# Performance work log

Hardware: AMD Instinct MI355X
Metric: run time of the kernel (lower is better)

Reference implementation:

```python
import jax, jax.numpy as jnp
import numpy as np

B, N, H = 8, 2000, 64  # batch, num_nodes(=input_dim), hidden(num_gru_units)


def _laplacian_self_loop(a):
    # batched: norm = D^{-1/2} (A + I) D^{-1/2}
    m = a + jnp.eye(a.shape[-1], dtype=a.dtype)
    d_inv_sqrt = jnp.sum(m, axis=-1) ** -0.5  # (B, N)
    return d_inv_sqrt[..., :, None] * m * d_inv_sqrt[..., None, :]


def _graph_conv(inputs, hidden_flat, adj, windd, W2, b2, W3, b3, W, b, out_dim):
    b_, _, n = inputs.shape
    # dynamic wind-based adjacency
    wind_now = inputs[:, 2, :] * 360.0  # (B, N)
    direction = jnp.abs(windd[None, :, :] - wind_now[:, :, None])  # (B, N, N)
    direction = jnp.where(direction > 360.0, 180.0, direction)
    d1 = jnp.maximum(jnp.cos(direction * (jnp.pi / 180.0)), 0.0)
    a = d1 @ W2.T + b2 + (adj @ W3.T + b3)[None]  # (B, N, N)
    a1 = _laplacian_self_loop(jnp.maximum(a, 0.0))
    # graph conv: concat [x, h] then A @ [.] then Linear
    x = jnp.concatenate([inputs[:, 0, :, None], hidden_flat.reshape(b_, n, H)], axis=2)  # (B,N,H+1)
    y = jnp.einsum('bij,bjh->bih', a1, x) @ W.T + b  # (B, N, out_dim)
    return y.reshape(b_, n * out_dim)


def reference(inputs, hidden_state, adj, windd, W2, b2, W3, b3, W1a, b1a, W1b, b1b, Wca1, Wca2, Wsa):
    b_, _, n = inputs.shape
    conc = _graph_conv(inputs, hidden_state, adj, windd, W2, b2, W3, b3, W1a, b1a, 2 * H)
    conc = conc.reshape(b_, 2 * H, n)  # faithful reshape (input_dim == N)
    # --- channel attention (CBAM) ---
    avg = jnp.mean(conc, axis=2, keepdims=True)  # (B, 2H, 1)
    mx = jnp.max(conc, axis=2, keepdims=True)
    def fc(v):
        return jnp.einsum('oc,bcx->box', Wca2, jax.nn.relu(jnp.einsum('oc,bcx->box', Wca1, v)))
    ca = jax.nn.sigmoid(fc(avg) + fc(mx))  # (B, 2H, 1)
    conc = ca * conc
    # --- spatial attention ---
    s = jnp.stack([jnp.mean(conc, axis=1), jnp.max(conc, axis=1)], axis=1)  # (B, 2, N)
    sa = jax.lax.conv_general_dilated(s, Wsa, window_strides=(1,), padding=((3, 3),),
                                      dimension_numbers=('NCH', 'OIH', 'NCH'))  # (B,1,N)
    conc = jax.nn.sigmoid(sa) * conc
    # --- GRU gates ---
    conc = jax.nn.sigmoid(conc.reshape(b_, 2 * H * n))
    r, u = jnp.split(conc, 2, axis=1)  # each (B, N*H)
    c = jnp.tanh(_graph_conv(inputs, r * hidden_state, adj, windd, W2, b2, W3, b3, W1b, b1b, H))
    new_hidden_state = u * hidden_state + (1.0 - u) * c
    return new_hidden_state


def setup_inputs() -> dict:
    key = jax.random.key(0)
    ks = jax.random.split(key, 12)
    inputs = jax.random.uniform(ks[0], (B, 3, N), dtype=jnp.float32)
    hidden_state = jax.random.normal(ks[1], (B, N * H), dtype=jnp.float32) * 0.1
    adj = jax.random.uniform(ks[2], (N, N), dtype=jnp.float32)
    windd = jax.random.uniform(ks[3], (N, N), dtype=jnp.float32) * 360.0
    sN = 1.0 / np.sqrt(N)
    W2 = jax.random.normal(ks[4], (N, N), dtype=jnp.float32) * sN
    b2 = jnp.zeros((N,), jnp.float32)
    W3 = jax.random.normal(ks[5], (N, N), dtype=jnp.float32) * sN
    b3 = jnp.zeros((N,), jnp.float32)
    sI = 1.0 / np.sqrt(H + 1)
    W1a = jax.random.normal(ks[6], (2 * H, H + 1), dtype=jnp.float32) * sI
    b1a = jnp.ones((2 * H,), jnp.float32)  # bias=1.0 in graph_conv1
    W1b = jax.random.normal(ks[7], (H, H + 1), dtype=jnp.float32) * sI
    b1b = jnp.zeros((H,), jnp.float32)
    Wca1 = jax.random.normal(ks[8], (2 * H // 16, 2 * H), dtype=jnp.float32) * (1.0 / np.sqrt(2 * H))
    Wca2 = jax.random.normal(ks[9], (2 * H, 2 * H // 16), dtype=jnp.float32) * (1.0 / np.sqrt(2 * H // 16))
    Wsa = jax.random.normal(ks[10], (1, 2, 7), dtype=jnp.float32) * (1.0 / np.sqrt(14))
    return {'inputs': inputs, 'hidden_state': hidden_state, 'adj': adj, 'windd': windd,
            'W2': W2, 'b2': b2, 'W3': W3, 'b3': b3, 'W1a': W1a, 'b1a': b1a,
            'W1b': W1b, 'b1b': b1b, 'Wca1': Wca1, 'Wca2': Wca2, 'Wsa': Wsa}
```

## Files before the change

kernel.cpp:

```cpp
#include <hip/hip_runtime.h>

#define NN 2000
#define BB 8
#define P  2048
#define NIT 32

typedef __attribute__((ext_vector_type(8))) short bf16x8;
typedef __attribute__((ext_vector_type(4))) float f32x4;

__device__ __forceinline__ float sigf(float x) { return 1.0f / (1.0f + expf(-x)); }

__device__ __forceinline__ short f2bf(float x) {
    union { float f; unsigned u; } v; v.f = x;
    unsigned r = v.u + 0x7fffu + ((v.u >> 16) & 1u);
    return (short)(r >> 16);
}
__device__ __forceinline__ float bf2f(short h) {
    union { unsigned u; float f; } v; v.u = ((unsigned)(unsigned short)h) << 16; return v.f;
}

__device__ __forceinline__ void gl2lds16(const short* g, short* l) {
    __builtin_amdgcn_global_load_lds(
        (const __attribute__((address_space(1))) void*)g,
        (__attribute__((address_space(3))) void*)l, 16, 0, 0);
}

__global__ __launch_bounds__(256) void k_cvtW(
    const float* __restrict__ s0, const float* __restrict__ s1, const float* __restrict__ s2,
    short* __restrict__ d0, short* __restrict__ d1, short* __restrict__ d2)
{
    const int i = blockIdx.x, sel = blockIdx.y, t = threadIdx.x;
    const float* s = (sel == 0) ? s0 : (sel == 1) ? s1 : s2;
    short* d = ((sel == 0) ? d0 : (sel == 1) ? d1 : d2) + ((size_t)i) * P + t * 8;
    bf16x8 v;
#pragma unroll
    for (int e = 0; e < 8; ++e) v[e] = 0;
    if (i < NN && t < 250) {
        const float* p = s + (size_t)i * NN + t * 8;
        float4 x0 = *(const float4*)p;
        float4 x1 = *(const float4*)(p + 4);
        float a[8] = {x0.x,x0.y,x0.z,x0.w,x1.x,x1.y,x1.z,x1.w};
#pragma unroll
        for (int e = 0; e < 8; ++e) v[e] = f2bf(a[e]);
    }
    *(bf16x8*)d = v;
}

__global__ __launch_bounds__(256) void k_cvtD1(
    const float* __restrict__ windd, const float* __restrict__ inputs, short* __restrict__ d1bf)
{
    const int i = blockIdx.x, t = threadIdx.x;
    const bool live = (i < NN) && (t < 250);
    float a[8];
    if (live) {
        const float* p = windd + (size_t)i * NN + t * 8;
        float4 x0 = *(const float4*)p;
        float4 x1 = *(const float4*)(p + 4);
        a[0]=x0.x; a[1]=x0.y; a[2]=x0.z; a[3]=x0.w;
        a[4]=x1.x; a[5]=x1.y; a[6]=x1.z; a[7]=x1.w;
    }
#pragma unroll
    for (int b = 0; b < BB; ++b) {
        bf16x8 v;
#pragma unroll
        for (int e = 0; e < 8; ++e) v[e] = 0;
        if (live) {
            const float wn = inputs[(size_t)b * 3 * NN + 2 * NN + i] * 360.0f;
#pragma unroll
            for (int e = 0; e < 8; ++e) {
                float dd = fabsf(a[e] - wn);
                dd = (dd > 360.0f) ? 180.0f : dd;
                float c = __cosf(dd * 0.01745329251994329577f);
                v[e] = f2bf(fmaxf(c, 0.0f));
            }
        }
        *(bf16x8*)(d1bf + ((size_t)b * P + i) * P + t * 8) = v;
    }
}

__global__ __launch_bounds__(512, 2) void k_gd(
    const short* __restrict__ d1bf, const short* __restrict__ W2bf,
    const float* __restrict__ b2, const short* __restrict__ adjw,
    short* __restrict__ m_bf)
{
    __shared__ char smem[131072];
    const int t = threadIdx.x;
    const int w = t >> 6, lane = t & 63;
    const int wm = w >> 2, wn = w & 3;
    const int lr = lane & 15, lq = lane >> 4;
    const int tile = blockIdx.x;
    const int b = blockIdx.y;
    const int i0 = (tile & 7) * 256;
    const int j0 = (tile >> 3) * 256;
    const short* A  = d1bf + (size_t)b * P * P;
    const short* Bm = W2bf;

    const short* srcA[4];
    const short* srcB[4];
#pragma unroll
    for (int q = 0; q < 4; ++q) {
        const int c = q * 512 + t;
        const int r = c >> 3;
        const int g = (c & 7) ^ (r & 7);
        srcA[q] = A  + (size_t)(i0 + r) * P + g * 8;
        srcB[q] = Bm + (size_t)(j0 + r) * P + g * 8;
    }

#define STAGE_ALL(slot, ktI) do {                                                      \
        gl2lds16(srcA[0] + (ktI) * 64, (short*)(smem + (slot) * 32768 + (w * 64) * 16));          \
        gl2lds16(srcA[1] + (ktI) * 64, (short*)(smem + (slot) * 32768 + (512 + w * 64) * 16));    \
        gl2lds16(srcA[2] + (ktI) * 64, (short*)(smem + (slot) * 32768 + (1024 + w * 64) * 16));   \
        gl2lds16(srcA[3] + (ktI) * 64, (short*)(smem + (slot) * 32768 + (1536 + w * 64) * 16));   \
        gl2lds16(srcB[0] + (ktI) * 64, (short*)(smem + 65536 + (slot) * 32768 + (w * 64) * 16));          \
        gl2lds16(srcB[1] + (ktI) * 64, (short*)(smem + 65536 + (slot) * 32768 + (512 + w * 64) * 16));    \
        gl2lds16(srcB[2] + (ktI) * 64, (short*)(smem + 65536 + (slot) * 32768 + (1024 + w * 64) * 16));   \
        gl2lds16(srcB[3] + (ktI) * 64, (short*)(smem + 65536 + (slot) * 32768 + (1536 + w * 64) * 16)); } while (0)

    const int fx0 = (lq << 4) ^ ((lr & 7) << 4);
    const int fx1 = ((4 + lq) << 4) ^ ((lr & 7) << 4);
    const int arowB = (wm * 128 + lr) * 128;
    const int browB = (wn * 64 + lr) * 128;

    f32x4 acc[8][4];
#pragma unroll
    for (int m = 0; m < 8; ++m)
#pragma unroll
        for (int n = 0; n < 4; ++n) acc[m][n] = (f32x4){0.f, 0.f, 0.f, 0.f};
    bf16x8 aF[4][2], bF[4][2];

    STAGE_ALL(0, 0);
    asm volatile("s_waitcnt vmcnt(0)" ::: "memory");
    __builtin_amdgcn_s_barrier();
    asm volatile("" ::: "memory");

#define MFMA_(a_, b_, m, n) acc[m][n] = __builtin_amdgcn_mfma_f32_16x16x32_bf16(a_, b_, acc[m][n], 0, 0, 0)

    for (int kt = 0; kt < NIT; ++kt) {
        char* curA = smem + (kt & 1) * 32768;
        char* curB = smem + 65536 + (kt & 1) * 32768;
        const int stgSlot = (kt + 1) & 1;
        const int stgKt = (kt + 1 < NIT) ? (kt + 1) : (NIT - 1);

        STAGE_ALL(stgSlot, stgKt);

#pragma unroll
        for (int m = 0; m < 4; ++m) {
            aF[m][0] = *(const bf16x8*)(curA + arowB + m * 2048 + fx0);
            aF[m][1] = *(const bf16x8*)(curA + arowB + m * 2048 + fx1);
        }
#pragma unroll
        for (int n = 0; n < 4; ++n) {
            bF[n][0] = *(const bf16x8*)(curB + browB + n * 2048 + fx0);
            bF[n][1] = *(const bf16x8*)(curB + browB + n * 2048 + fx1);
        }
        asm volatile("s_waitcnt lgkmcnt(0)" ::: "memory");
        __builtin_amdgcn_sched_barrier(0);
        __builtin_amdgcn_s_setprio(1);
#pragma unroll
        for (int m = 0; m < 4; ++m)
#pragma unroll
            for (int n = 0; n < 4; ++n) {
                MFMA_(aF[m][0], bF[n][0], m, n);
                MFMA_(aF[m][1], bF[n][1], m, n);
            }
        __builtin_amdgcn_s_setprio(0);

#pragma unroll
        for (int m = 0; m < 4; ++m) {
            aF[m][0] = *(const bf16x8*)(curA + arowB + (m + 4) * 2048 + fx0);
            aF[m][1] = *(const bf16x8*)(curA + arowB + (m + 4) * 2048 + fx1);
        }
        asm volatile("s_waitcnt lgkmcnt(0)" ::: "memory");
        __builtin_amdgcn_sched_barrier(0);
        __builtin_amdgcn_s_setprio(1);
#pragma unroll
        for (int m = 0; m < 4; ++m)
#pragma unroll
            for (int n = 0; n < 4; ++n) {
                MFMA_(aF[m][0], bF[n][0], m + 4, n);
                MFMA_(aF[m][1], bF[n][1], m + 4, n);
            }
        __builtin_amdgcn_s_setprio(0);

        asm volatile("s_waitcnt vmcnt(0)" ::: "memory");
        __builtin_amdgcn_s_barrier();
        asm volatile("" ::: "memory");
    }

    const int rbase = i0 + wm * 128 + lq * 4;
    const int cbase = j0 + wn * 64 + lr;
#pragma unroll
    for (int m = 0; m < 8; ++m) {
#pragma unroll
        for (int n = 0; n < 4; ++n) {
            const int col = cbase + n * 16;
#pragma unroll
            for (int q = 0; q < 4; ++q) {
                const int row = rbase + m * 16 + q;
                short o = 0;
                if (row < NN && col < NN) {
                    float x = acc[m][n][q] + b2[col] + bf2f(adjw[(size_t)row * NN + col]);
                    x = fmaxf(x, 0.0f);
                    if (row == col) x += 1.0f;
                    o = f2bf(x);
                }
                m_bf[((size_t)b * P + row) * P + col] = o;
            }
        }
    }
#undef MFMA_
#undef STAGE_ALL
}

template<int EPI, int OUTD>
__global__ __launch_bounds__(256) void k_mfma(
    const short* __restrict__ Abase, const short* __restrict__ Bbase,
    const float* __restrict__ bias, const short* __restrict__ adjw,
    void* __restrict__ Cout, short* __restrict__ part, size_t aBatch)
{
    __shared__ short shA[4096];
    __shared__ short shB[4096];
    const int t = threadIdx.x;
    const int w = t >> 6, lane = t & 63;
    const int wr = w >> 1, wc = w & 1;

    int i0, j0, b, kt = 0;
    if (EPI == 2) {
        i0 = blockIdx.x * 128; j0 = 0; kt = blockIdx.y; b = blockIdx.z;
    } else {
        i0 = blockIdx.x * 128; j0 = blockIdx.y * 128; b = 0;
    }
    const int kb = (EPI == 2) ? kt * (P / 4) : 0;
    const int ke = (EPI == 2) ? kt * (P / 4) + (P / 4) : P;

    const short* A  = Abase + (size_t)b * aBatch;
    const short* Bm = Bbase + ((EPI == 2) ? (size_t)b * 128 * P : (size_t)0);

    f32x4 acc[4][4];
#pragma unroll
    for (int m = 0; m < 4; ++m)
#pragma unroll
        for (int n = 0; n < 4; ++n) acc[m][n] = (f32x4){0.f, 0.f, 0.f, 0.f};

    const int lidx0 = w * 128 + lane;
    const int lidx1 = lidx0 + 64;
    const short* aS0 = A  + (size_t)(i0 + (lidx0 >> 2)) * P + (lidx0 & 3) * 8;
    const short* aS1 = A  + (size_t)(i0 + (lidx1 >> 2)) * P + (lidx1 & 3) * 8;
    const short* bS0 = Bm + (size_t)(j0 + (lidx0 >> 2)) * P + (lidx0 & 3) * 8;
    const short* bS1 = Bm + (size_t)(j0 + (lidx1 >> 2)) * P + (lidx1 & 3) * 8;
    short* ldA0 = shA + (w * 128) * 8;
    short* ldA1 = shA + (w * 128 + 64) * 8;
    short* ldB0 = shB + (w * 128) * 8;
    short* ldB1 = shB + (w * 128 + 64) * 8;

    const int lr = lane & 15, lq = lane >> 4;
    const int aoff = (wr * 64 + lr) * 32 + lq * 8;
    const int boff = (wc * 64 + lr) * 32 + lq * 8;

    for (int k0 = kb; k0 < ke; k0 += 32) {
        gl2lds16(aS0 + k0, ldA0);
        gl2lds16(aS1 + k0, ldA1);
        gl2lds16(bS0 + k0, ldB0);
        gl2lds16(bS1 + k0, ldB1);
        __syncthreads();
        bf16x8 aF[4], bF[4];
#pragma unroll
        for (int m = 0; m < 4; ++m) aF[m] = *(const bf16x8*)(shA + aoff + m * 512);
#pragma unroll
        for (int n = 0; n < 4; ++n) bF[n] = *(const bf16x8*)(shB + boff + n * 512);
#pragma unroll
        for (int m = 0; m < 4; ++m)
#pragma unroll
            for (int n = 0; n < 4; ++n)
                acc[m][n] = __builtin_amdgcn_mfma_f32_16x16x32_bf16(aF[m], bF[n], acc[m][n], 0, 0, 0);
        __syncthreads();
    }

    const int rbase = i0 + wr * 64 + lq * 4;
    const int cbase = j0 + wc * 64 + lr;
#pragma unroll
    for (int m = 0; m < 4; ++m) {
#pragma unroll
        for (int n = 0; n < 4; ++n) {
            const int col = cbase + n * 16;
#pragma unroll
            for (int q = 0; q < 4; ++q) {
                const int row = rbase + m * 16 + q;
                float v = acc[m][n][q];
                if (EPI == 0) {
                    if (row < NN && col < NN)
                        ((short*)Cout)[(size_t)row * NN + col] = f2bf(v + bias[col]);
                } else {
                    if (row < NN && col < OUTD)
                        part[((size_t)(kt * BB + b) * NN + row) * OUTD + col] = f2bf(v);
                }
            }
        }
    }
}

template<int OUTD>
__global__ __launch_bounds__(256) void k_comb(
    const short* __restrict__ part, const float* __restrict__ dinv,
    const float* __restrict__ bias, float* __restrict__ out)
{
    const size_t idx = (size_t)blockIdx.x * 256 + threadIdx.x;
    const size_t S = (size_t)BB * NN * OUTD;
    if (idx >= S) return;
    const int o = (int)(idx % OUTD);
    const size_t r = idx / OUTD;
    const int i = (int)(r % NN);
    const int b = (int)(r / NN);
    float s = (bf2f(part[idx]) + bf2f(part[idx + S])) +
              (bf2f(part[idx + 2 * S]) + bf2f(part[idx + 3 * S]));
    out[idx] = s * dinv[b * NN + i] + bias[o];
}

__global__ __launch_bounds__(256) void k_cfin(
    const short* __restrict__ part, const float* __restrict__ dinv,
    const float* __restrict__ bias, const float* __restrict__ u,
    const float* __restrict__ hidden, float* __restrict__ out)
{
    const size_t idx = (size_t)blockIdx.x * 256 + threadIdx.x;
    const size_t S = (size_t)BB * NN * 64;
    if (idx >= S) return;
    const int o = (int)(idx & 63);
    const size_t r = idx >> 6;
    const int i = (int)(r % NN);
    const int b = (int)(r / NN);
    float s = (bf2f(part[idx]) + bf2f(part[idx + S])) +
              (bf2f(part[idx + 2 * S]) + bf2f(part[idx + 3 * S]));
    float c = tanhf(s * dinv[b * NN + i] + bias[o]);
    float uu = u[idx];
    out[idx] = uu * hidden[idx] + (1.0f - uu) * c;
}

__global__ __launch_bounds__(256) void k_rowsum_bf(const short* __restrict__ m_bf, float* __restrict__ dinv)
{
    const int i = blockIdx.x, b = blockIdx.y;
    const short* p = m_bf + ((size_t)b * P + i) * P + threadIdx.x * 8;
    bf16x8 v = *(const bf16x8*)p;
    float s = 0.0f;
#pragma unroll
    for (int e = 0; e < 8; ++e) s += bf2f(v[e]);
#pragma unroll
    for (int off = 32; off > 0; off >>= 1) s += __shfl_down(s, off);
    __shared__ float red[4];
    if ((threadIdx.x & 63) == 0) red[threadIdx.x >> 6] = s;
    __syncthreads();
    if (threadIdx.x == 0) dinv[b * NN + i] = rsqrtf(red[0] + red[1] + red[2] + red[3]);
}

template<int OUT>
__global__ __launch_bounds__(128) void k_xwT(
    const float* __restrict__ inputs, const float* __restrict__ hsrc,
    const float* __restrict__ W, const float* __restrict__ dinv, short* __restrict__ zT)
{
    const int b = blockIdx.y;
    const int j0 = blockIdx.x * 16;
    const int t = threadIdx.x;
    __shared__ float wl[128 * 65];
    __shared__ float xs[16 * 66];
    __shared__ float dj[16];
    for (int idx = t; idx < OUT * 65; idx += 128) wl[idx] = W[idx];
    for (int idx = t; idx < 16 * 64; idx += 128) {
        int jj = idx >> 6, hh = idx & 63, j = j0 + jj;
        xs[jj * 66 + 1 + hh] = (j < NN) ? hsrc[((size_t)b * NN + j) * 64 + hh] : 0.0f;
    }
    if (t < 16) {
        int j = j0 + t;
        xs[t * 66] = (j < NN) ? inputs[(size_t)b * 3 * NN + j] : 0.0f;
        dj[t] = (j < NN) ? dinv[b * NN + j] : 0.0f;
    }
    __syncthreads();
    for (int jj = 0; jj < 16; ++jj) {
        float a = 0.0f;
        if (t < OUT) {
            const float* xr = &xs[jj * 66];
            const float* wr = &wl[t * 65];
#pragma unroll
            for (int c = 0; c < 65; ++c) a = fmaf(xr[c], wr[c], a);
        }
        int j = j0 + jj;
        zT[((size_t)b * 128 + t) * P + j] = (t < OUT && j < NN) ? f2bf(a * dj[jj]) : (short)0;
    }
}

__global__ __launch_bounds__(256) void k_chred(const float* __restrict__ conc,
                                               float* __restrict__ avg, float* __restrict__ mx)
{
    const int bc = blockIdx.x;
    const float* p = conc + (size_t)bc * NN;
    float s = 0.0f, mv = -3.402823466e+38f;
    for (int n = threadIdx.x; n < NN; n += 256) { float v = p[n]; s += v; mv = fmaxf(mv, v); }
#pragma unroll
    for (int off = 32; off > 0; off >>= 1) {
        s += __shfl_down(s, off);
        mv = fmaxf(mv, __shfl_down(mv, off));
    }
    __shared__ float rs[4], rm[4];
    if ((threadIdx.x & 63) == 0) { rs[threadIdx.x >> 6] = s; rm[threadIdx.x >> 6] = mv; }
    __syncthreads();
    if (threadIdx.x == 0) {
        avg[bc] = (rs[0] + rs[1] + rs[2] + rs[3]) * (1.0f / NN);
        mx[bc]  = fmaxf(fmaxf(rm[0], rm[1]), fmaxf(rm[2], rm[3]));
    }
}

__global__ __launch_bounds__(128) void k_ca(
    const float* __restrict__ avg, const float* __restrict__ mx,
    const float* __restrict__ Wca1, const float* __restrict__ Wca2, float* __restrict__ ca)
{
    const int b = blockIdx.x, t = threadIdx.x;
    __shared__ float av[128], mv[128], h[16];
    av[t] = avg[b * 128 + t];
    mv[t] = mx[b * 128 + t];
    __syncthreads();
    if (t < 16) {
        int o8 = t & 7;
        const float* src = (t < 8) ? av : mv;
        float s = 0.0f;
        for (int c = 0; c < 128; ++c) s = fmaf(Wca1[o8 * 128 + c], src[c], s);
        h[t] = fmaxf(s, 0.0f);
    }
    __syncthreads();
    float s = 0.0f;
#pragma unroll
    for (int k = 0; k < 8; ++k) s = fmaf(Wca2[t * 8 + k], h[k] + h[8 + k], s);
    ca[b * 128 + t] = sigf(s);
}

__global__ __launch_bounds__(256) void k_satgate(
    const float* __restrict__ conc, const float* __restrict__ ca,
    const float* __restrict__ Wsa, const float* __restrict__ hidden,
    float* __restrict__ rh, float* __restrict__ u)
{
    const int b = blockIdx.y;
    const int n0 = blockIdx.x * 256;
    const int t = threadIdx.x;
    __shared__ float cas[128];
    __shared__ float wsa[14];
    __shared__ float s0l[262], s1l[262];
    if (t < 128) cas[t] = ca[b * 128 + t];
    if (t >= 128 && t < 142) wsa[t - 128] = Wsa[t - 128];
    __syncthreads();

    const float* cb = conc + (size_t)b * NN * 128;
    {
        const int n = n0 + t;
        float sm = 0.0f, sx = -3.402823466e+38f;
        if (n < NN) {
            for (int c = 0; c < 128; ++c) {
                float v = cas[c] * cb[(size_t)c * NN + n];
                sm += v; sx = fmaxf(sx, v);
            }
            s0l[t + 3] = sm * (1.0f / 128.0f);
            s1l[t + 3] = sx;
        } else { s0l[t + 3] = 0.0f; s1l[t + 3] = 0.0f; }
    }
    if (t < 6) {
        const int hn = (t < 3) ? (n0 - 3 + t) : (n0 + 256 + (t - 3));
        const int hi = (t < 3) ? t : (256 + t);
        float sm = 0.0f, sx = -3.402823466e+38f;
        if (hn >= 0 && hn < NN) {
            for (int c = 0; c < 128; ++c) {
                float v = cas[c] * cb[(size_t)c * NN + hn];
                sm += v; sx = fmaxf(sx, v);
            }
            s0l[hi] = sm * (1.0f / 128.0f);
            s1l[hi] = sx;
        } else { s0l[hi] = 0.0f; s1l[hi] = 0.0f; }
    }
    __syncthreads();

    const int n = n0 + t;
    if (n >= NN) return;
    float sa = 0.0f;
#pragma unroll
    for (int k = 0; k < 7; ++k)
        sa += wsa[k] * s0l[t + k] + wsa[7 + k] * s1l[t + k];
    float gs = sigf(sa);
    for (int c = 0; c < 128; ++c) {
        float v = gs * cas[c] * cb[(size_t)c * NN + n];
        float g = sigf(v);
        if (c < 64)
            rh[(size_t)b * NN * 64 + (size_t)c * NN + n] =
                g * hidden[(size_t)b * NN * 64 + (size_t)c * NN + n];
        else
            u[(size_t)b * NN * 64 + (size_t)(c - 64) * NN + n] = g;
    }
}

extern "C" void kernel_launch(void* const* d_in, const int* in_sizes, int n_in,
                              void* d_out, int out_size, void* d_ws, size_t ws_size,
                              hipStream_t stream)
{
    (void)in_sizes; (void)n_in; (void)out_size; (void)ws_size;
    const float* inputs = (const float*)d_in[0];
    const float* hidden = (const float*)d_in[1];
    const float* adj    = (const float*)d_in[2];
    const float* windd  = (const float*)d_in[3];
    const float* W2     = (const float*)d_in[4];
    const float* b2     = (const float*)d_in[5];
    const float* W3     = (const float*)d_in[6];
    const float* b3     = (const float*)d_in[7];
    const float* W1a    = (const float*)d_in[8];
    const float* b1a    = (const float*)d_in[9];
    const float* W1b    = (const float*)d_in[10];
    const float* b1b    = (const float*)d_in[11];
    const float* Wca1   = (const float*)d_in[12];
    const float* Wca2   = (const float*)d_in[13];
    const float* Wsa    = (const float*)d_in[14];
    float* out = (float*)d_out;

    char* W = (char*)d_ws;
    short* adjW3bf = (short*)(W + 0);
    short* W2bf    = (short*)(W + 8000000);
    short* W3bf    = (short*)(W + 16388608);
    short* adjbf   = (short*)(W + 24777216);
    short* m_bf    = (short*)(W + 16388608);
    char* D = W + 83497472;
    short* d1bf = (short*)D;
    float* dinv = (float*)(D + 0);
    float* avgb = (float*)(D + 64000);
    float* mxb  = (float*)(D + 68096);
    float* cab  = (float*)(D + 72192);
    short* zT   = (short*)(D + 204800);
    float* conc = (float*)(D + 4399104);
    float* rh   = (float*)(D + 12591104);
    float* ubuf = (float*)(D + 16687104);
    short* part = (short*)(D + 24879104);

    const size_t PP = (size_t)P * P;

    k_cvtW<<<dim3(P, 3), 256, 0, stream>>>(W2, W3, adj, W2bf, W3bf, adjbf);
    k_cvtD1<<<P, 256, 0, stream>>>(windd, inputs, d1bf);
    k_mfma<0, 0><<<dim3(16, 16, 1), 256, 0, stream>>>(adjbf, W3bf, b3, nullptr, adjW3bf, nullptr, 0);
    k_gd<<<dim3(64, BB), 512, 0, stream>>>(d1bf, W2bf, b2, adjW3bf, m_bf);
    k_rowsum_bf<<<dim3(NN, BB), 256, 0, stream>>>(m_bf, dinv);
    k_xwT<128><<<dim3(128, BB), 128, 0, stream>>>(inputs, hidden, W1a, dinv, zT);
    k_mfma<2, 128><<<dim3(16, 4, BB), 256, 0, stream>>>(m_bf, zT, nullptr, nullptr, nullptr, part, PP);
    k_comb<128><<<(BB * NN * 128 + 255) / 256, 256, 0, stream>>>(part, dinv, b1a, conc);
    k_chred<<<BB * 128, 256, 0, stream>>>(conc, avgb, mxb);
    k_ca<<<BB, 128, 0, stream>>>(avgb, mxb, Wca1, Wca2, cab);
    k_satgate<<<dim3(8, BB), 256, 0, stream>>>(conc, cab, Wsa, hidden, rh, ubuf);
    k_xwT<64><<<dim3(128, BB), 128, 0, stream>>>(inputs, rh, W1b, dinv, zT);
    k_mfma<2, 64><<<dim3(16, 4, BB), 256, 0, stream>>>(m_bf, zT, nullptr, nullptr, nullptr, part, PP);
    k_cfin<<<(BB * NN * 64 + 255) / 256, 256, 0, stream>>>(part, dinv, b1b, ubuf, hidden, out);
}
```

Measured before the change: 411.9 us.

## Restructure dynamic-adjacency GEMM into four-stage K=32 LDS pipeline with prefetch depth two

The main batched d1@W2 GEMM kernel now uses K-tiles of 32 instead of 64, with four LDS slots and loads issued two tiles ahead. Each iteration waits only on the older tile's loads (vmcnt(4)) rather than draining all outstanding loads. This is meant to hide global-to-LDS latency behind the MFMA work. The cost is twice as many barriers per K, a new swizzle pattern and more live fragment registers (8 A fragments at once).

```diff
diff --git a/kernel.cpp b/kernel.cpp
--- a/kernel.cpp
+++ b/kernel.cpp
@@ -3,7 +3,7 @@
 #define NN 2000
 #define BB 8
 #define P  2048
-#define NIT 32
+#define NIT4 64
 
 typedef __attribute__((ext_vector_type(8))) short bf16x8;
 typedef __attribute__((ext_vector_type(4))) float f32x4;
@@ -78,7 +78,7 @@
     }
 }
 
-__global__ __launch_bounds__(512, 2) void k_gd(
+__global__ __launch_bounds__(512, 2) void k_gq(
     const short* __restrict__ d1bf, const short* __restrict__ W2bf,
     const float* __restrict__ b2, const short* __restrict__ adjw,
     short* __restrict__ m_bf)
@@ -95,97 +95,62 @@
     const short* A  = d1bf + (size_t)b * P * P;
     const short* Bm = W2bf;
 
-    const short* srcA[4];
-    const short* srcB[4];
-#pragma unroll
-    for (int q = 0; q < 4; ++q) {
-        const int c = q * 512 + t;
-        const int r = c >> 3;
-        const int g = (c & 7) ^ (r & 7);
-        srcA[q] = A  + (size_t)(i0 + r) * P + g * 8;
-        srcB[q] = Bm + (size_t)(j0 + r) * P + g * 8;
-    }
-
-#define STAGE_ALL(slot, ktI) do {                                                      \
-        gl2lds16(srcA[0] + (ktI) * 64, (short*)(smem + (slot) * 32768 + (w * 64) * 16));          \
-        gl2lds16(srcA[1] + (ktI) * 64, (short*)(smem + (slot) * 32768 + (512 + w * 64) * 16));    \
-        gl2lds16(srcA[2] + (ktI) * 64, (short*)(smem + (slot) * 32768 + (1024 + w * 64) * 16));   \
-        gl2lds16(srcA[3] + (ktI) * 64, (short*)(smem + (slot) * 32768 + (1536 + w * 64) * 16));   \
-        gl2lds16(srcB[0] + (ktI) * 64, (short*)(smem + 65536 + (slot) * 32768 + (w * 64) * 16));          \
-        gl2lds16(srcB[1] + (ktI) * 64, (short*)(smem + 65536 + (slot) * 32768 + (512 + w * 64) * 16));    \
-        gl2lds16(srcB[2] + (ktI) * 64, (short*)(smem + 65536 + (slot) * 32768 + (1024 + w * 64) * 16));   \
-        gl2lds16(srcB[3] + (ktI) * 64, (short*)(smem + 65536 + (slot) * 32768 + (1536 + w * 64) * 16)); } while (0)
-
-    const int fx0 = (lq << 4) ^ ((lr & 7) << 4);
-    const int fx1 = ((4 + lq) << 4) ^ ((lr & 7) << 4);
-    const int arowB = (wm * 128 + lr) * 128;
-    const int browB = (wn * 64 + lr) * 128;
+    const int c0 = t,       r0 = c0 >> 2;
+    const int c1 = 512 + t, r1 = c1 >> 2;
+    const int g0 = (c0 & 3) ^ ((r0 >> 1) & 3);
+    const int g1 = (c1 & 3) ^ ((r1 >> 1) & 3);
+    const short* srcA0 = A  + (size_t)(i0 + r0) * P + g0 * 8;
+    const short* srcA1 = A  + (size_t)(i0 + r1) * P + g1 * 8;
+    const short* srcB0 = Bm + (size_t)(j0 + r0) * P + g0 * 8;
+    const short* srcB1 = Bm + (size_t)(j0 + r1) * P + g1 * 8;
+
+#define STAGE4(slot, ktI) do {                                                          \
+        gl2lds16(srcA0 + (ktI) * 32, (short*)(smem + (slot) * 16384 + t * 16));         \
+        gl2lds16(srcA1 + (ktI) * 32, (short*)(smem + (slot) * 16384 + 8192 + t * 16));  \
+        gl2lds16(srcB0 + (ktI) * 32, (short*)(smem + 65536 + (slot) * 16384 + t * 16)); \
+        gl2lds16(srcB1 + (ktI) * 32, (short*)(smem + 65536 + (slot) * 16384 + 8192 + t * 16)); } while (0)
+
+    const int fx = ((lq ^ ((lr >> 1) & 3)) << 4);
+    const int arowB = (wm * 128 + lr) * 64;
+    const int browB = (wn * 64 + lr) * 64;
 
     f32x4 acc[8][4];
 #pragma unroll
     for (int m = 0; m < 8; ++m)
 #pragma unroll
         for (int n = 0; n < 4; ++n) acc[m][n] = (f32x4){0.f, 0.f, 0.f, 0.f};
-    bf16x8 aF[4][2], bF[4][2];
-
-    STAGE_ALL(0, 0);
-    asm volatile("s_waitcnt vmcnt(0)" ::: "memory");
+
+    STAGE4(0, 0);
+    STAGE4(1, 1);
+    asm volatile("s_waitcnt vmcnt(4)" ::: "memory");
     __builtin_amdgcn_s_barrier();
     asm volatile("" ::: "memory");
 
-#define MFMA_(a_, b_, m, n) acc[m][n] = __builtin_amdgcn_mfma_f32_16x16x32_bf16(a_, b_, acc[m][n], 0, 0, 0)
-
-    for (int kt = 0; kt < NIT; ++kt) {
-        char* curA = smem + (kt & 1) * 32768;
-        char* curB = smem + 65536 + (kt & 1) * 32768;
-        const int stgSlot = (kt + 1) & 1;
-        const int stgKt = (kt + 1 < NIT) ? (kt + 1) : (NIT - 1);
-
-        STAGE_ALL(stgSlot, stgKt);
-
-#pragma unroll
-        for (int m = 0; m < 4; ++m) {
-            aF[m][0] = *(const bf16x8*)(curA + arowB + m * 2048 + fx0);
-            aF[m][1] = *(const bf16x8*)(curA + arowB + m * 2048 + fx1);
-        }
-#pragma unroll
-        for (int n = 0; n < 4; ++n) {
-            bF[n][0] = *(const bf16x8*)(curB + browB + n * 2048 + fx0);
-            bF[n][1] = *(const bf16x8*)(curB + browB + n * 2048 + fx1);
-        }
-        asm volatile("s_waitcnt lgkmcnt(0)" ::: "memory");
-        __builtin_amdgcn_sched_barrier(0);
+    for (int kt = 0; kt < NIT4; ++kt) {
+        char* curA = smem + (kt & 3) * 16384;
+        char* curB = smem + 65536 + (kt & 3) * 16384;
+        const int stgKt = (kt + 2 < NIT4) ? (kt + 2) : kt;
+        STAGE4((kt + 2) & 3, stgKt);
+
+        bf16x8 aF[8], bF[4];
+#pragma unroll
+        for (int m = 0; m < 8; ++m) aF[m] = *(const bf16x8*)(curA + arowB + m * 1024 + fx);
+#pragma unroll
+        for (int n = 0; n < 4; ++n) bF[n] = *(const bf16x8*)(curB + browB + n * 1024 + fx);
+
         __builtin_amdgcn_s_setprio(1);
 #pragma unroll
-        for (int m = 0; m < 4; ++m)
-#pragma unroll
-            for (int n = 0; n < 4; ++n) {
-                MFMA_(aF[m][0], bF[n][0], m, n);
-                MFMA_(aF[m][1], bF[n][1], m, n);
-            }
+        for (int m = 0; m < 8; ++m)
+#pragma unroll
+            for (int n = 0; n < 4; ++n)
+                acc[m][n] = __builtin_amdgcn_mfma_f32_16x16x32_bf16(aF[m], bF[n], acc[m][n], 0, 0, 0);
         __builtin_amdgcn_s_setprio(0);
 
-#pragma unroll
-        for (int m = 0; m < 4; ++m) {
-            aF[m][0] = *(const bf16x8*)(curA + arowB + (m + 4) * 2048 + fx0);
-            aF[m][1] = *(const bf16x8*)(curA + arowB + (m + 4) * 2048 + fx1);
-        }
-        asm volatile("s_waitcnt lgkmcnt(0)" ::: "memory");
-        __builtin_amdgcn_sched_barrier(0);
-        __builtin_amdgcn_s_setprio(1);
-#pragma unroll
-        for (int m = 0; m < 4; ++m)
-#pragma unroll
-            for (int n = 0; n < 4; ++n) {
-                MFMA_(aF[m][0], bF[n][0], m + 4, n);
-                MFMA_(aF[m][1], bF[n][1], m + 4, n);
-            }
-        __builtin_amdgcn_s_setprio(0);
-
-        asm volatile("s_waitcnt vmcnt(0)" ::: "memory");
+        asm volatile("s_waitcnt vmcnt(4)" ::: "memory");
         __builtin_amdgcn_s_barrier();
         asm volatile("" ::: "memory");
     }
+    asm volatile("s_waitcnt vmcnt(0)" ::: "memory");
 
     const int rbase = i0 + wm * 128 + lq * 4;
     const int cbase = j0 + wn * 64 + lr;
@@ -208,8 +173,7 @@
             }
         }
     }
-#undef MFMA_
-#undef STAGE_ALL
+#undef STAGE4
 }
 
 template<int EPI, int OUTD>
@@ -536,7 +500,7 @@
     k_cvtW<<<dim3(P, 3), 256, 0, stream>>>(W2, W3, adj, W2bf, W3bf, adjbf);
     k_cvtD1<<<P, 256, 0, stream>>>(windd, inputs, d1bf);
     k_mfma<0, 0><<<dim3(16, 16, 1), 256, 0, stream>>>(adjbf, W3bf, b3, nullptr, adjW3bf, nullptr, 0);
-    k_gd<<<dim3(64, BB), 512, 0, stream>>>(d1bf, W2bf, b2, adjW3bf, m_bf);
+    k_gq<<<dim3(64, BB), 512, 0, stream>>>(d1bf, W2bf, b2, adjW3bf, m_bf);
     k_rowsum_bf<<<dim3(NN, BB), 256, 0, stream>>>(m_bf, dinv);
     k_xwT<128><<<dim3(128, BB), 128, 0, stream>>>(inputs, hidden, W1a, dinv, zT);
     k_mfma<2, 128><<<dim3(16, 4, BB), 256, 0, stream>>>(m_bf, zT, nullptr, nullptr, nullptr, part, PP);
```

Result: no change. 419.5 us (+1.9%).
